# Kernel tuning notes

Hardware: AMD Instinct MI355X
Metric: run time of the kernel (lower is better)

Reference implementation:

```python
import jax, jax.numpy as jnp
import numpy as np

EMBED = 1024
HEADS = 16
DH = EMBED // HEADS
B, S = 2, 2048


def setup_inputs() -> dict:
    key = jax.random.key(0)
    ks = jax.random.split(key, 12)
    inp = {
        "k": jax.random.normal(ks[0], (B, S, EMBED), jnp.float32),
        "q": jax.random.normal(ks[1], (B, S, EMBED), jnp.float32),
        "v": jax.random.normal(ks[2], (B, S, EMBED), jnp.float32),
        "mask": jax.random.randint(ks[3], (B, 1, S, S), 0, 2, jnp.int32),
        # per-head projections (shared across heads, as in the torch module)
        "Wk": jax.random.normal(ks[4], (DH, DH), jnp.float32) / np.sqrt(DH),
        "bk": jnp.zeros((DH,), jnp.float32),
        "Wq": jax.random.normal(ks[5], (DH, DH), jnp.float32) / np.sqrt(DH),
        "bq": jnp.zeros((DH,), jnp.float32),
        "Wv": jax.random.normal(ks[6], (DH, DH), jnp.float32) / np.sqrt(DH),
        "bv": jnp.zeros((DH,), jnp.float32),
        "Wo": jax.random.normal(ks[7], (EMBED, EMBED), jnp.float32) / np.sqrt(EMBED),
        "bo": jnp.zeros((EMBED,), jnp.float32),
    }
    return inp


def reference(k, q, v, mask, Wk, bk, Wq, bq, Wv, bv, Wo, bo):
    b, s, _ = k.shape
    sq = q.shape[1]
    # [B,S,H,dh]
    kh = k.reshape(b, s, HEADS, DH)
    qh = q.reshape(b, sq, HEADS, DH)
    vh = v.reshape(b, s, HEADS, DH)
    # per-head linear (weight shared across heads): x @ W.T + b
    kh = kh @ Wk.T + bk
    qh = qh @ Wq.T + bq
    vh = vh @ Wv.T + bv
    # scores [B,H,Sq,Sk]
    product = jnp.einsum("bqhd,bkhd->bhqk", qh, kh)
    # masked_fill BEFORE scaling, as in the original
    product = jnp.where(mask == 0, jnp.float32(-1e20), product)
    product = product / np.sqrt(DH)
    scores = jax.nn.softmax(product, axis=-1)
    ctx = jnp.einsum("bhqk,bkhd->bqhd", scores, vh).reshape(b, sq, EMBED)
    return ctx @ Wo.T + bo
```

## Files before the change

### kernel.cpp

```cpp
#include <hip/hip_runtime.h>
#include <hip/hip_bf16.h>
#include <math.h>

#define EMBED 1024
#define HEADS 16
#define DH    64
#define BATCH 2
#define SEQ   2048

typedef __attribute__((ext_vector_type(8))) short bf16x8;
typedef __attribute__((ext_vector_type(4))) short bf16x4;
typedef __attribute__((ext_vector_type(4))) float f32x4;
typedef unsigned long long u64;

#define QSCALE 0.1803368801111244f

static __device__ __forceinline__ unsigned short f2bf(float x) {
    unsigned u = __builtin_bit_cast(unsigned, x);
    return (unsigned short)((u + 0x7fffu + ((u >> 16) & 1u)) >> 16);
}
static __device__ __forceinline__ unsigned pk2bf(float a, float b) {
    union { __hip_bfloat162 h2; unsigned u; } c;
    c.h2 = __float22bfloat162_rn(make_float2(a, b));
    return c.u;
}
static __device__ __forceinline__ float fexp2(float x) {
#if __has_builtin(__builtin_amdgcn_exp2f)
    return __builtin_amdgcn_exp2f(x);
#else
    float r; asm("v_exp_f32 %0, %1" : "=v"(r) : "v"(x)); return r;
#endif
}
static __device__ __forceinline__ void gl_lds16(const void* g, void* l) {
    __builtin_amdgcn_global_load_lds(
        (const __attribute__((address_space(1))) void*)g,
        (__attribute__((address_space(3))) void*)l, 16, 0, 0);
}
static __device__ __forceinline__ bf16x8 cvt8(const float* p) {
    float4 a = ((const float4*)p)[0];
    float4 b = ((const float4*)p)[1];
    union { unsigned u[4]; bf16x8 v; } c;
    c.u[0] = pk2bf(a.x, a.y); c.u[1] = pk2bf(a.z, a.w);
    c.u[2] = pk2bf(b.x, b.y); c.u[3] = pk2bf(b.z, b.w);
    return c.v;
}

__global__ __launch_bounds__(256) void proj_mfma(
    const float* __restrict__ q, const float* __restrict__ k, const float* __restrict__ v,
    const float* __restrict__ Wq, const float* __restrict__ bq,
    const float* __restrict__ Wk, const float* __restrict__ bk,
    const float* __restrict__ Wv, const float* __restrict__ bv,
    unsigned short* __restrict__ qh, unsigned short* __restrict__ kh,
    unsigned short* __restrict__ vt,
    const int* __restrict__ mask, u64* __restrict__ bits,
    const float* __restrict__ Wo, unsigned short* __restrict__ Wob)
{
    const int blk   = blockIdx.x;
    const int which = blockIdx.y;
    const int t     = threadIdx.x;

    if (which == 3) {
        if (blk < 512) {
            const int idx = blk * 256 + t;
            const int4* src = (const int4*)(mask + (size_t)idx * 64);
            u64 wb = 0;
#pragma unroll
            for (int u = 0; u < 16; ++u) {
                int4 m = src[u];
                u64 nib = (m.x != 0 ? 1ull : 0) | (m.y != 0 ? 2ull : 0) |
                          (m.z != 0 ? 4ull : 0) | (m.w != 0 ? 8ull : 0);
                wb |= nib << (u * 4);
            }
            bits[idx] = wb;
        } else {
            const int i = ((blk - 512) * 256 + t) * 8;
            float4 a = ((const float4*)(Wo + i))[0];
            float4 b = ((const float4*)(Wo + i))[1];
            unsigned o32[4] = {pk2bf(a.x, a.y), pk2bf(a.z, a.w),
                               pk2bf(b.x, b.y), pk2bf(b.z, b.w)};
            *(uint4*)(Wob + i) = *(uint4*)o32;
        }
        return;
    }

    const float* x; const float* W; const float* bias;
    if (which == 0)      { x = q; W = Wq; bias = bq; }
    else if (which == 1) { x = k; W = Wk; bias = bk; }
    else                 { x = v; W = Wv; bias = bv; }

    __shared__ unsigned short Ws[64 * 72];

    const int w    = t >> 6;
    const int lane = t & 63;
    const int l15  = lane & 15;
    const int quad = lane >> 4;

    const int sr = t >> 2, sp = t & 3;
    {
        const float* wsrc = W + (size_t)sr * 64 + sp * 16;
        unsigned o32[8];
#pragma unroll
        for (int u4 = 0; u4 < 4; ++u4) {
            float4 a = ((const float4*)wsrc)[u4];
            o32[u4 * 2 + 0] = pk2bf(a.x, a.y);
            o32[u4 * 2 + 1] = pk2bf(a.z, a.w);
        }
        *(uint4*)&Ws[sr * 72 + sp * 16]     = *(uint4*)&o32[0];
        *(uint4*)&Ws[sr * 72 + sp * 16 + 8] = *(uint4*)&o32[4];
    }

    if (which == 2) {
        const int bh = blk >> 5;
        const int st = blk & 31;
        const int b  = bh >> 4, h = bh & 15;
        const int s  = st * 64 + w * 16 + l15;

        const float* xrow = x + ((size_t)(b * SEQ + s)) * EMBED + h * DH;
        const bf16x8 bx0 = cvt8(xrow + quad * 8);
        const bf16x8 bx1 = cvt8(xrow + 32 + quad * 8);

        __syncthreads();

#pragma unroll
        for (int nt = 0; nt < 4; ++nt) {
            bf16x8 aw0 = *(const bf16x8*)&Ws[(nt * 16 + l15) * 72 + quad * 8];
            bf16x8 aw1 = *(const bf16x8*)&Ws[(nt * 16 + l15) * 72 + 32 + quad * 8];
            f32x4 a = {0, 0, 0, 0};
            a = __builtin_amdgcn_mfma_f32_16x16x32_bf16(aw0, bx0, a, 0, 0, 0);
            a = __builtin_amdgcn_mfma_f32_16x16x32_bf16(aw1, bx1, a, 0, 0, 0);
#pragma unroll
            for (int r = 0; r < 4; ++r) {
                const int d = nt * 16 + quad * 4 + r;
                vt[((size_t)bh * DH + d) * SEQ + s] = f2bf(a[r] + bias[d]);
            }
        }
        return;
    }

    const float oscale = (which == 0) ? QSCALE : 1.0f;
    unsigned short* out = (which == 0) ? qh : kh;

    const float* xrow = x + ((size_t)blk * 64 + w * 16 + l15) * 64;
    const bf16x8 af0 = cvt8(xrow + quad * 8);
    const bf16x8 af1 = cvt8(xrow + 32 + quad * 8);

    __syncthreads();

    f32x4 acc[4];
#pragma unroll
    for (int nt = 0; nt < 4; ++nt) {
        bf16x8 bf0 = *(const bf16x8*)&Ws[(nt * 16 + l15) * 72 + quad * 8];
        bf16x8 bf1 = *(const bf16x8*)&Ws[(nt * 16 + l15) * 72 + 32 + quad * 8];
        f32x4 a = {0, 0, 0, 0};
        a = __builtin_amdgcn_mfma_f32_16x16x32_bf16(af0, bf0, a, 0, 0, 0);
        a = __builtin_amdgcn_mfma_f32_16x16x32_bf16(af1, bf1, a, 0, 0, 0);
        acc[nt] = a;
    }

    const int bsidx = blk * 4 + w;
    const int b = bsidx >> 11, s = bsidx & 2047;
#pragma unroll
    for (int nt = 0; nt < 4; ++nt) {
        const int d = nt * 16 + l15;
        const float bb = bias[d];
#pragma unroll
        for (int r = 0; r < 4; ++r) {
            const int h = quad * 4 + r;
            out[(((size_t)b * HEADS + h) * SEQ + s) * DH + d] =
                f2bf((acc[nt][r] + bb) * oscale);
        }
    }
}

__global__ __launch_bounds__(512, 4) void attn_kernel(
    const unsigned short* __restrict__ qh, const unsigned short* __restrict__ kh,
    const unsigned short* __restrict__ vt, const u64* __restrict__ mbits,
    unsigned short* __restrict__ ctx)
{
    const int bid = blockIdx.x;
    const int bh  = bid & 31;
    const int q0  = (bid >> 5) * 128;
    const int b   = bh >> 4;

    __shared__ unsigned char smem[65536];

    const int t    = threadIdx.x;
    const int w    = t >> 6;
    const int lane = t & 63;
    const int l15  = lane & 15;
    const int quad = lane >> 4;

    const int srow   = lane >> 3;
    const int schunk = (lane & 7) ^ srow;

    const unsigned short* qb = qh + ((size_t)bh * SEQ + q0 + w * 16 + l15) * DH + quad * 8;
    const bf16x8 qf0 = *(const bf16x8*)qb;
    const bf16x8 qf1 = *(const bf16x8*)(qb + 32);

    f32x4 O[4];
#pragma unroll
    for (int dt = 0; dt < 4; ++dt) O[dt] = f32x4{0, 0, 0, 0};
    f32x4 Osum = {0, 0, 0, 0};
    const bf16x4 ones = {(short)0x3F80, (short)0x3F80, (short)0x3F80, (short)0x3F80};

    const unsigned short* kbase = kh + (size_t)bh * SEQ * DH
                                  + (size_t)srow * DH + schunk * 8;
    const unsigned short* vbase = vt + (size_t)bh * DH * SEQ
                                  + (size_t)srow * SEQ + schunk * 8;
    const u64* mrow = mbits + ((size_t)b * SEQ + q0 + w * 16 + l15) * (SEQ / 64);

    auto stage = [&](int kp, unsigned char* buf) {
#pragma unroll
        for (int j = 0; j < 4; ++j) {
            const int idx = w * 4 + j;
            if (idx < 16) {
                const int u = idx >> 3, i = idx & 7;
                gl_lds16(kbase + ((size_t)kp * 128 + u * 64 + i * 8) * DH,
                         buf + u * 8192 + i * 1024);
            } else {
                const int u = (idx - 16) >> 3, i = (idx - 16) & 7;
                gl_lds16(vbase + kp * 128 + u * 64 + (size_t)i * 8 * SEQ,
                         buf + 16384 + u * 8192 + i * 1024);
            }
        }
    };

    stage(0, smem);
    u64 pm0 = mrow[0], pm1 = mrow[1];
    __syncthreads();

    for (int it = 0; it < 16; ++it) {
        if (it < 15) stage(it + 1, smem + ((it + 1) & 1) * 32768);
        const u64 mb0 = pm0, mb1 = pm1;
        if (it < 15) { pm0 = mrow[2 * it + 2]; pm1 = mrow[2 * it + 3]; }

        const unsigned char* buf = smem + (it & 1) * 32768;

        __builtin_amdgcn_s_setprio(1);
#pragma unroll
        for (int u = 0; u < 2; ++u) {
            const unsigned short* KtH = (const unsigned short*)(buf + u * 8192);
            const unsigned short* VtH = (const unsigned short*)(buf + 16384 + u * 8192);
            const u64 mq = (u ? mb1 : mb0) >> (quad * 4);

            bf16x4 p[4];
            const int rx = l15 & 7;
#pragma unroll
            for (int st = 0; st < 4; ++st) {
                const int r = st * 16 + l15;
                bf16x8 kf0 = *(const bf16x8*)&KtH[r * 64 + ((quad ^ rx)) * 8];
                bf16x8 kf1 = *(const bf16x8*)&KtH[r * 64 + ((quad ^ rx) ^ 4) * 8];
                f32x4 sa = {0, 0, 0, 0};
                sa = __builtin_amdgcn_mfma_f32_16x16x32_bf16(kf0, qf0, sa, 0, 0, 0);
                sa = __builtin_amdgcn_mfma_f32_16x16x32_bf16(kf1, qf1, sa, 0, 0, 0);
                const unsigned nib = (unsigned)(mq >> (st * 16)) & 0xFu;
                float p0 = (nib & 1u) ? fexp2(sa[0]) : 0.f;
                float p1 = (nib & 2u) ? fexp2(sa[1]) : 0.f;
                float p2 = (nib & 4u) ? fexp2(sa[2]) : 0.f;
                float p3 = (nib & 8u) ? fexp2(sa[3]) : 0.f;
                union { unsigned u2[2]; bf16x4 v; } pu;
                pu.u2[0] = pk2bf(p0, p1);
                pu.u2[1] = pk2bf(p2, p3);
                p[st] = pu.v;
                Osum = __builtin_amdgcn_mfma_f32_16x16x16bf16_1k(p[st], ones, Osum, 0, 0, 0);
            }

#pragma unroll
            for (int dt = 0; dt < 4; ++dt) {
                const int d = dt * 16 + l15;
                const int dx = l15 & 7;
#pragma unroll
                for (int st = 0; st < 4; ++st) {
                    const int ch = (st * 2 + (quad >> 1)) ^ dx;
                    bf16x4 vb = *(const bf16x4*)&VtH[d * 64 + ch * 8 + (quad & 1) * 4];
                    O[dt] = __builtin_amdgcn_mfma_f32_16x16x16bf16_1k(p[st], vb, O[dt], 0, 0, 0);
                }
            }
        }
        __builtin_amdgcn_s_setprio(0);
        __syncthreads();
    }

    float inv[4];
#pragma unroll
    for (int r = 0; r < 4; ++r) inv[r] = 1.0f / Osum[r];
#pragma unroll
    for (int r = 0; r < 4; ++r) {
        const int row = q0 + w * 16 + quad * 4 + r;
        unsigned short* dst = ctx + ((size_t)bh * SEQ + row) * DH + l15;
#pragma unroll
        for (int dt = 0; dt < 4; ++dt)
            dst[dt * 16] = f2bf(O[dt][r] * inv[r]);
    }
}

__global__ __launch_bounds__(256, 4) void outproj_mfma(
    const unsigned short* __restrict__ ctx, const unsigned short* __restrict__ Wob,
    const float* __restrict__ bo, float* __restrict__ out)
{
    const int n0 = blockIdx.x * 64;
    const int m0 = blockIdx.y * 64;
    const int b  = m0 / SEQ;
    const int s0 = m0 % SEQ;

    __shared__ unsigned char smem[32768];

    const int t    = threadIdx.x;
    const int w    = t >> 6;
    const int lane = t & 63;
    const int l15  = lane & 15;
    const int quad = lane >> 4;
    const int srow   = lane >> 3;
    const int schunk = (lane & 7) ^ srow;

    const unsigned short* abase = ctx + ((size_t)b * HEADS * SEQ + s0 + srow) * DH + schunk * 8;
    const unsigned short* wbase = Wob + (size_t)(n0 + srow) * EMBED + schunk * 8;

    f32x4 acc[4] = {f32x4{0,0,0,0}, f32x4{0,0,0,0}, f32x4{0,0,0,0}, f32x4{0,0,0,0}};

    {
        unsigned char* Ab = smem;
        unsigned char* Wb = smem + 8192;
#pragma unroll
        for (int j = 0; j < 4; ++j) {
            const int idx = w * 4 + j;
            if (idx < 8)
                gl_lds16(abase + (size_t)idx * 8 * DH, Ab + idx * 1024);
            else
                gl_lds16(wbase + (size_t)(idx - 8) * 8 * EMBED, Wb + (idx - 8) * 1024);
        }
    }
    __syncthreads();

    for (int kt = 0; kt < 16; ++kt) {
        if (kt < 15) {
            const int ktn = kt + 1;
            unsigned char* Ab = smem + (ktn & 1) * 16384;
            unsigned char* Wb = Ab + 8192;
#pragma unroll
            for (int j = 0; j < 4; ++j) {
                const int idx = w * 4 + j;
                if (idx < 8)
                    gl_lds16(abase + (size_t)ktn * SEQ * DH + (size_t)idx * 8 * DH,
                             Ab + idx * 1024);
                else
                    gl_lds16(wbase + (size_t)(idx - 8) * 8 * EMBED + ktn * 64,
                             Wb + (idx - 8) * 1024);
            }
        }

        const unsigned short* At = (const unsigned short*)(smem + (kt & 1) * 16384);
        const unsigned short* Wt = At + 4096;
        const int rx = l15 & 7;
        const int c0 = ((quad ^ rx)) * 8;

        bf16x8 bf0 = *(const bf16x8*)&Wt[(w * 16 + l15) * 64 + c0];
        bf16x8 bf1 = *(const bf16x8*)&Wt[(w * 16 + l15) * 64 + (c0 ^ 32)];
#pragma unroll
        for (int mt = 0; mt < 4; ++mt) {
            bf16x8 af0 = *(const bf16x8*)&At[(mt * 16 + l15) * 64 + c0];
            bf16x8 af1 = *(const bf16x8*)&At[(mt * 16 + l15) * 64 + (c0 ^ 32)];
            acc[mt] = __builtin_amdgcn_mfma_f32_16x16x32_bf16(af0, bf0, acc[mt], 0, 0, 0);
            acc[mt] = __builtin_amdgcn_mfma_f32_16x16x32_bf16(af1, bf1, acc[mt], 0, 0, 0);
        }
        __syncthreads();
    }

    const float bv = bo[n0 + w * 16 + l15];
#pragma unroll
    for (int mt = 0; mt < 4; ++mt) {
#pragma unroll
        for (int r = 0; r < 4; ++r) {
            out[(size_t)(m0 + mt * 16 + quad * 4 + r) * EMBED + n0 + w * 16 + l15] =
                acc[mt][r] + bv;
        }
    }
}

extern "C" void kernel_launch(void* const* d_in, const int* in_sizes, int n_in,
                              void* d_out, int out_size, void* d_ws, size_t ws_size,
                              hipStream_t stream) {
    const float* k    = (const float*)d_in[0];
    const float* q    = (const float*)d_in[1];
    const float* v    = (const float*)d_in[2];
    const int*   mask = (const int*)  d_in[3];
    const float* Wk   = (const float*)d_in[4];
    const float* bk   = (const float*)d_in[5];
    const float* Wq   = (const float*)d_in[6];
    const float* bq   = (const float*)d_in[7];
    const float* Wv   = (const float*)d_in[8];
    const float* bv   = (const float*)d_in[9];
    const float* Wo   = (const float*)d_in[10];
    const float* bo   = (const float*)d_in[11];
    float* out = (float*)d_out;

    const size_t TEN = (size_t)BATCH * HEADS * SEQ * DH;
    unsigned short* qh_bf = (unsigned short*)d_ws;
    unsigned short* kh_bf = qh_bf + TEN;
    unsigned short* vt_bf = kh_bf + TEN;
    unsigned short* ctxb  = vt_bf + TEN;
    unsigned short* Wob   = ctxb + TEN;
    u64*            mbits = (u64*)(Wob + EMBED * EMBED);

    proj_mfma<<<dim3(1024, 4), 256, 0, stream>>>(
        q, k, v, Wq, bq, Wk, bk, Wv, bv,
        qh_bf, kh_bf, vt_bf, mask, mbits, Wo, Wob);
    attn_kernel<<<dim3((SEQ / 128) * BATCH * HEADS), 512, 0, stream>>>(
        qh_bf, kh_bf, vt_bf, mbits, ctxb);
    outproj_mfma<<<dim3(EMBED / 64, BATCH * SEQ / 64), 256, 0, stream>>>(
        ctxb, Wob, bo, out);
}
```

Baseline: 216.2 us.

## Process two query row-groups per wave in attention, halving block threads

Each wave in the attention kernel now handles 32 query rows, two 16-row groups, instead of 16, and the block shrinks from 512 to 256 threads. Each K fragment and V fragment read from LDS is reused across both query groups, which halves LDS read traffic per unit of MFMA work. Each wave also stages twice as many tiles. The cost is roughly double the accumulator and register state per wave, and fewer waves per CU for hiding latency. Launch bounds change to (256,2).

```diff
diff --git a/kernel.cpp b/kernel.cpp
--- a/kernel.cpp
+++ b/kernel.cpp
@@ -172,7 +172,7 @@
     }
 }
 
-__global__ __launch_bounds__(512, 4) void attn_kernel(
+__global__ __launch_bounds__(256, 2) void attn_kernel(
     const unsigned short* __restrict__ qh, const unsigned short* __restrict__ kh,
     const unsigned short* __restrict__ vt, const u64* __restrict__ mbits,
     unsigned short* __restrict__ ctx)
@@ -193,26 +193,34 @@
     const int srow   = lane >> 3;
     const int schunk = (lane & 7) ^ srow;
 
-    const unsigned short* qb = qh + ((size_t)bh * SEQ + q0 + w * 16 + l15) * DH + quad * 8;
-    const bf16x8 qf0 = *(const bf16x8*)qb;
-    const bf16x8 qf1 = *(const bf16x8*)(qb + 32);
-
-    f32x4 O[4];
-#pragma unroll
-    for (int dt = 0; dt < 4; ++dt) O[dt] = f32x4{0, 0, 0, 0};
-    f32x4 Osum = {0, 0, 0, 0};
+    bf16x8 qf[2][2];
+#pragma unroll
+    for (int g = 0; g < 2; ++g) {
+        const unsigned short* qb =
+            qh + ((size_t)bh * SEQ + q0 + w * 32 + g * 16 + l15) * DH + quad * 8;
+        qf[g][0] = *(const bf16x8*)qb;
+        qf[g][1] = *(const bf16x8*)(qb + 32);
+    }
+
+    f32x4 O[2][4];
+#pragma unroll
+    for (int g = 0; g < 2; ++g)
+#pragma unroll
+        for (int dt = 0; dt < 4; ++dt) O[g][dt] = f32x4{0, 0, 0, 0};
+    f32x4 Osum[2] = {f32x4{0, 0, 0, 0}, f32x4{0, 0, 0, 0}};
     const bf16x4 ones = {(short)0x3F80, (short)0x3F80, (short)0x3F80, (short)0x3F80};
 
     const unsigned short* kbase = kh + (size_t)bh * SEQ * DH
                                   + (size_t)srow * DH + schunk * 8;
     const unsigned short* vbase = vt + (size_t)bh * DH * SEQ
                                   + (size_t)srow * SEQ + schunk * 8;
-    const u64* mrow = mbits + ((size_t)b * SEQ + q0 + w * 16 + l15) * (SEQ / 64);
+    const u64* mrow0 = mbits + ((size_t)b * SEQ + q0 + w * 32 + l15) * (SEQ / 64);
+    const u64* mrow1 = mrow0 + 16 * (SEQ / 64);
 
     auto stage = [&](int kp, unsigned char* buf) {
 #pragma unroll
-        for (int j = 0; j < 4; ++j) {
-            const int idx = w * 4 + j;
+        for (int j = 0; j < 8; ++j) {
+            const int idx = w * 8 + j;
             if (idx < 16) {
                 const int u = idx >> 3, i = idx & 7;
                 gl_lds16(kbase + ((size_t)kp * 128 + u * 64 + i * 8) * DH,
@@ -226,13 +234,17 @@
     };
 
     stage(0, smem);
-    u64 pm0 = mrow[0], pm1 = mrow[1];
+    u64 pm[2][2] = {{mrow0[0], mrow0[1]}, {mrow1[0], mrow1[1]}};
     __syncthreads();
 
     for (int it = 0; it < 16; ++it) {
         if (it < 15) stage(it + 1, smem + ((it + 1) & 1) * 32768);
-        const u64 mb0 = pm0, mb1 = pm1;
-        if (it < 15) { pm0 = mrow[2 * it + 2]; pm1 = mrow[2 * it + 3]; }
+        const u64 mb00 = pm[0][0], mb01 = pm[0][1];
+        const u64 mb10 = pm[1][0], mb11 = pm[1][1];
+        if (it < 15) {
+            pm[0][0] = mrow0[2 * it + 2]; pm[0][1] = mrow0[2 * it + 3];
+            pm[1][0] = mrow1[2 * it + 2]; pm[1][1] = mrow1[2 * it + 3];
+        }
 
         const unsigned char* buf = smem + (it & 1) * 32768;
 
@@ -241,28 +253,34 @@
         for (int u = 0; u < 2; ++u) {
             const unsigned short* KtH = (const unsigned short*)(buf + u * 8192);
             const unsigned short* VtH = (const unsigned short*)(buf + 16384 + u * 8192);
-            const u64 mq = (u ? mb1 : mb0) >> (quad * 4);
-
-            bf16x4 p[4];
+            const u64 mq0 = (u ? mb01 : mb00) >> (quad * 4);
+            const u64 mq1 = (u ? mb11 : mb10) >> (quad * 4);
+
+            bf16x4 p[2][4];
             const int rx = l15 & 7;
 #pragma unroll
             for (int st = 0; st < 4; ++st) {
                 const int r = st * 16 + l15;
                 bf16x8 kf0 = *(const bf16x8*)&KtH[r * 64 + ((quad ^ rx)) * 8];
                 bf16x8 kf1 = *(const bf16x8*)&KtH[r * 64 + ((quad ^ rx) ^ 4) * 8];
-                f32x4 sa = {0, 0, 0, 0};
-                sa = __builtin_amdgcn_mfma_f32_16x16x32_bf16(kf0, qf0, sa, 0, 0, 0);
-                sa = __builtin_amdgcn_mfma_f32_16x16x32_bf16(kf1, qf1, sa, 0, 0, 0);
-                const unsigned nib = (unsigned)(mq >> (st * 16)) & 0xFu;
-                float p0 = (nib & 1u) ? fexp2(sa[0]) : 0.f;
-                float p1 = (nib & 2u) ? fexp2(sa[1]) : 0.f;
-                float p2 = (nib & 4u) ? fexp2(sa[2]) : 0.f;
-                float p3 = (nib & 8u) ? fexp2(sa[3]) : 0.f;
-                union { unsigned u2[2]; bf16x4 v; } pu;
-                pu.u2[0] = pk2bf(p0, p1);
-                pu.u2[1] = pk2bf(p2, p3);
-                p[st] = pu.v;
-                Osum = __builtin_amdgcn_mfma_f32_16x16x16bf16_1k(p[st], ones, Osum, 0, 0, 0);
+#pragma unroll
+                for (int g = 0; g < 2; ++g) {
+                    f32x4 sa = {0, 0, 0, 0};
+                    sa = __builtin_amdgcn_mfma_f32_16x16x32_bf16(kf0, qf[g][0], sa, 0, 0, 0);
+                    sa = __builtin_amdgcn_mfma_f32_16x16x32_bf16(kf1, qf[g][1], sa, 0, 0, 0);
+                    const unsigned nib =
+                        (unsigned)((g ? mq1 : mq0) >> (st * 16)) & 0xFu;
+                    float p0 = (nib & 1u) ? fexp2(sa[0]) : 0.f;
+                    float p1 = (nib & 2u) ? fexp2(sa[1]) : 0.f;
+                    float p2 = (nib & 4u) ? fexp2(sa[2]) : 0.f;
+                    float p3 = (nib & 8u) ? fexp2(sa[3]) : 0.f;
+                    union { unsigned u2[2]; bf16x4 v; } pu;
+                    pu.u2[0] = pk2bf(p0, p1);
+                    pu.u2[1] = pk2bf(p2, p3);
+                    p[g][st] = pu.v;
+                    Osum[g] = __builtin_amdgcn_mfma_f32_16x16x16bf16_1k(
+                        p[g][st], ones, Osum[g], 0, 0, 0);
+                }
             }
 
 #pragma unroll
@@ -273,7 +291,10 @@
                 for (int st = 0; st < 4; ++st) {
                     const int ch = (st * 2 + (quad >> 1)) ^ dx;
                     bf16x4 vb = *(const bf16x4*)&VtH[d * 64 + ch * 8 + (quad & 1) * 4];
-                    O[dt] = __builtin_amdgcn_mfma_f32_16x16x16bf16_1k(p[st], vb, O[dt], 0, 0, 0);
+                    O[0][dt] = __builtin_amdgcn_mfma_f32_16x16x16bf16_1k(
+                        p[0][st], vb, O[0][dt], 0, 0, 0);
+                    O[1][dt] = __builtin_amdgcn_mfma_f32_16x16x16bf16_1k(
+                        p[1][st], vb, O[1][dt], 0, 0, 0);
                 }
             }
         }
@@ -281,16 +302,19 @@
         __syncthreads();
     }
 
-    float inv[4];
-#pragma unroll
-    for (int r = 0; r < 4; ++r) inv[r] = 1.0f / Osum[r];
-#pragma unroll
-    for (int r = 0; r < 4; ++r) {
-        const int row = q0 + w * 16 + quad * 4 + r;
-        unsigned short* dst = ctx + ((size_t)bh * SEQ + row) * DH + l15;
-#pragma unroll
-        for (int dt = 0; dt < 4; ++dt)
-            dst[dt * 16] = f2bf(O[dt][r] * inv[r]);
+#pragma unroll
+    for (int g = 0; g < 2; ++g) {
+        float inv[4];
+#pragma unroll
+        for (int r = 0; r < 4; ++r) inv[r] = 1.0f / Osum[g][r];
+#pragma unroll
+        for (int r = 0; r < 4; ++r) {
+            const int row = q0 + w * 32 + g * 16 + quad * 4 + r;
+            unsigned short* dst = ctx + ((size_t)bh * SEQ + row) * DH + l15;
+#pragma unroll
+            for (int dt = 0; dt < 4; ++dt)
+                dst[dt * 16] = f2bf(O[g][dt][r] * inv[r]);
+        }
     }
 }
 
@@ -405,7 +429,7 @@
     proj_mfma<<<dim3(1024, 4), 256, 0, stream>>>(
         q, k, v, Wq, bq, Wk, bk, Wv, bv,
         qh_bf, kh_bf, vt_bf, mask, mbits, Wo, Wob);
-    attn_kernel<<<dim3((SEQ / 128) * BATCH * HEADS), 512, 0, stream>>>(
+    attn_kernel<<<dim3((SEQ / 128) * BATCH * HEADS), 256, 0, stream>>>(
         qh_bf, kh_bf, vt_bf, mbits, ctxb);
     outproj_mfma<<<dim3(EMBED / 64, BATCH * SEQ / 64), 256, 0, stream>>>(
         ctxb, Wob, bo, out);
```

Result: no change. 220.3 us (+1.9%).
